# Performance work log

Measured on AMD Instinct MI355X. Metric: run time of the kernel, lower is better.

The kernel has to match this reference:

```python
import jax, jax.numpy as jnp
import numpy as np

B, N, H, V, STEP = 16, 50, 128, 40000, 2

def setup_inputs() -> dict:
    key = jax.random.key(0)
    ks = jax.random.split(key, 24)
    def nrm(i, shape, s=0.08):
        return jax.random.normal(ks[i], shape, jnp.float32) * s
    items = jax.random.randint(ks[0], (B, N), 0, V)
    A = jax.random.uniform(ks[1], (B, N, 2 * N), jnp.float32)
    lengths = jax.random.randint(ks[2], (B,), 1, N + 1)
    mask = (jnp.arange(N)[None, :] < lengths[:, None]).astype(jnp.int32)
    emb = nrm(3, (V, H), 0.1).at[0].set(0.0)  # padding_idx=0 row zeroed
    return dict(
        items=items, A=A, mask=mask, emb=emb,
        w_ih=nrm(4, (3 * H, 2 * H)), w_hh=nrm(5, (3 * H, H)),
        b_ih=nrm(6, (3 * H,)), b_hh=nrm(7, (3 * H,)),
        b_iah=nrm(8, (H,)), b_oah=nrm(9, (H,)),
        W_ein=nrm(10, (H, H)), b_ein=nrm(11, (H,)),
        W_eout=nrm(12, (H, H)), b_eout=nrm(13, (H,)),
        W_one=nrm(14, (H, H)), b_one=nrm(15, (H,)),
        W_two=nrm(16, (H, H)), b_two=nrm(17, (H,)),
        w_three=nrm(18, (H,)),
        W_tr=nrm(19, (H, 2 * H)), b_tr=nrm(20, (H,)),
        W_t=nrm(21, (H, H)),
    )

def gnn_cell(A, hidden, w_ih, w_hh, b_ih, b_hh, b_iah, b_oah, W_ein, b_ein, W_eout, b_eout):
    # A: [B,N,2N], hidden: [B,N,H]
    ein = hidden @ W_ein.T + b_ein
    eout = hidden @ W_eout.T + b_eout
    input_in = jnp.einsum('bnm,bmh->bnh', A[:, :, :N], ein) + b_iah
    input_out = jnp.einsum('bnm,bmh->bnh', A[:, :, N:], eout) + b_oah
    inputs = jnp.concatenate([input_in, input_out], axis=-1)  # [B,N,2H]
    gi = inputs @ w_ih.T + b_ih
    gh = hidden @ w_hh.T + b_hh
    i_r, i_i, i_n = jnp.split(gi, 3, axis=-1)
    h_r, h_i, h_n = jnp.split(gh, 3, axis=-1)
    resetgate = jax.nn.sigmoid(i_r + h_r)
    inputgate = jax.nn.sigmoid(i_i + h_i)
    newgate = jnp.tanh(i_n + resetgate * h_n)
    return newgate + inputgate * (hidden - newgate)

def reference(items, A, mask, emb, w_ih, w_hh, b_ih, b_hh, b_iah, b_oah,
              W_ein, b_ein, W_eout, b_eout, W_one, b_one, W_two, b_two,
              w_three, W_tr, b_tr, W_t):
    hidden = emb[items]  # [B,N,H]
    for _ in range(STEP):
        hidden = gnn_cell(A, hidden, w_ih, w_hh, b_ih, b_hh, b_iah, b_oah,
                          W_ein, b_ein, W_eout, b_eout)
    # compute_scores
    lengths = jnp.sum(mask, axis=1)  # all >= 1 by construction
    ht = hidden[jnp.arange(B), lengths - 1]  # [B,H] last valid item
    q1 = (ht @ W_one.T + b_one)[:, None, :]
    q2 = hidden @ W_two.T + b_two
    mexp = mask[..., None].astype(jnp.float32)  # [B,N,1]
    alpha_logits = jax.nn.sigmoid(q1 + q2) @ w_three[:, None]  # [B,N,1]
    alpha = jax.nn.softmax(jnp.where(mexp == 0, -jnp.inf, alpha_logits), axis=1)
    a = jnp.sum(alpha * hidden * mexp, axis=1)  # [B,H]
    a = jnp.concatenate([a, ht], axis=1) @ W_tr.T + b_tr  # hybrid (nonhybrid=False)
    b_emb = emb[1:]  # [V-1,H]
    qt = (hidden * mexp) @ W_t.T  # [B,N,H]
    beta_logits = jnp.einsum('vh,bnh->bvn', b_emb, qt)
    beta_logits = jnp.where(mask[:, None, :] == 0, -jnp.inf, beta_logits)
    beta = jax.nn.softmax(beta_logits, axis=-1)  # [B,V-1,N]
    target = jnp.einsum('bvn,bnh->bvh', beta, qt * mexp)  # [B,V-1,H]
    # scores = sum((a[:,None,:] + target) * b_emb, -1), split to avoid extra buffer
    scores = jnp.einsum('bvh,vh->bv', target, b_emb) + a @ b_emb.T
    return scores  # [B, V-1]
```

## Files before the change

### kernel.cpp

```cpp
#include <hip/hip_runtime.h>

#define BB 16
#define NN 50
#define HH 128
#define VV 40000
#define VO 39999

typedef unsigned short u16;
typedef unsigned int u32;
typedef __attribute__((ext_vector_type(8))) short short8;
typedef __attribute__((ext_vector_type(4))) float f32x4;

#define OFF_HID    0
#define OFF_HID2   102400
#define OFF_Q2     102400
#define OFF_Q1     204800
#define OFF_HT     206848
#define OFF_QTBF   307200
#define OFF_LEN    411648
#define OFF_WTWOT  591888
#define OFF_WTT    608272
#define OFF_WONET  624656
#define OFF_WTRT   641040

__device__ __forceinline__ float sigm(float x){ return 1.0f/(1.0f+__expf(-x)); }
__device__ __forceinline__ float b2f(u16 u){
  union { u32 i; float f; } c; c.i = ((u32)u) << 16; return c.f;
}
__device__ __forceinline__ u16 f2b(float f){
  union { float f; u32 i; } c; c.f = f;
  u32 u = c.i;
  return (u16)((u + 0x7fffu + ((u >> 16) & 1u)) >> 16);
}
__device__ __forceinline__ int frag_idx(int b, int n, int k){
  int tile = n>>4, vlo = n&15, kc = k>>5, quad = (k>>3)&3, j = k&7;
  return (((b*4+tile)*4+kc)<<9) + ((quad<<4)+vlo)*8 + j;
}

__global__ void k_pre(const int* __restrict__ items, const float* __restrict__ emb,
                      const float* __restrict__ W_two, const float* __restrict__ W_t,
                      const float* __restrict__ W_one, const float* __restrict__ W_tr,
                      float* __restrict__ ws){
  int idx = blockIdx.x*256 + threadIdx.x;
  if (idx < 102400){
    int r = idx >> 7, h = idx & 127;
    ws[OFF_HID + idx] = emb[items[r]*128 + h];
  } else if (idx < 118784){
    int i = idx-102400; int k=i>>7, h=i&127;
    ws[OFF_WTWOT + i] = W_two[h*128 + k];
  } else if (idx < 135168){
    int i = idx-118784; int k=i>>7, h=i&127;
    ws[OFF_WTT + i] = W_t[h*128 + k];
  } else if (idx < 151552){
    int i = idx-135168; int k=i>>7, h=i&127;
    ws[OFF_WONET + i] = W_one[h*128 + k];
  } else if (idx < 184320){
    int i = idx-151552; int k=i>>7, h=i&127;
    ws[OFF_WTRT + i] = W_tr[h*256 + k];
  }
}

__global__ void __launch_bounds__(384) k_step(const float* __restrict__ A,
                       const float* __restrict__ w_ih, const float* __restrict__ w_hh,
                       const float* __restrict__ W_ein, const float* __restrict__ W_eout,
                       const float* __restrict__ b_ein, const float* __restrict__ b_eout,
                       const float* __restrict__ b_iah, const float* __restrict__ b_oah,
                       const float* __restrict__ b_ih, const float* __restrict__ b_hh,
                       float* __restrict__ ws, int srcOff, int dstOff){
  __shared__ float hall[50][128];
  __shared__ float arow[2][104];
  __shared__ float hAl[2][256];
  __shared__ float sAl[2][2];
  __shared__ float inp[2][256];
  __shared__ float gil[2][384];
  __shared__ float ghl[2][384];
  int t = threadIdx.x;
  int tile = blockIdx.x, b = blockIdx.y;
  int n0 = tile*2;
  const float* hsrc = ws + srcOff + b*6400;
  for (int o=t; o<1600; o+=384) ((float4*)hall)[o] = ((const float4*)hsrc)[o];
  for (int o=t; o<208; o+=384){
    int r=o/104, c=o-r*104;
    arow[r][c] = (c<100) ? A[(size_t)(b*NN+n0+r)*100 + c] : 0.0f;
  }
  __syncthreads();
  for (int o=t; o<512; o+=384){
    int r = o>>8, kk = o&255;
    int k = kk & 127;
    const float* ar = &arow[r][(kk>>7)*50];
    float acc = 0.0f;
    #pragma unroll 5
    for (int m=0;m<50;m++) acc += ar[m]*hall[m][k];
    hAl[r][kk] = acc;
  }
  if (t < 4){
    int r = t>>1, half = t&1;
    const float* ar = &arow[r][half*50];
    float s = 0.0f;
    for (int m=0;m<50;m++) s += ar[m];
    sAl[r][half] = s;
  }
  __syncthreads();
  for (int o=t; o<512; o+=384){
    int r = o>>8, c8 = o&255;
    int in_half = (c8 < 128);
    int c = c8 & 127;
    const float* wrow = (in_half ? W_ein : W_eout) + c*128;
    const float* hv = &hAl[r][in_half ? 0 : 128];
    float acc = in_half ? (b_iah[c] + sAl[r][0]*b_ein[c])
                        : (b_oah[c] + sAl[r][1]*b_eout[c]);
    #pragma unroll 8
    for (int k=0;k<128;k+=4){
      float4 w4 = *(const float4*)(wrow + k);
      float4 h4 = *(const float4*)(hv + k);
      acc += h4.x*w4.x + h4.y*w4.y + h4.z*w4.z + h4.w*w4.w;
    }
    inp[r][c8] = acc;
  }
  __syncthreads();
  {
    int j = t;
    float gi0=b_ih[j], gi1=gi0, gh0=b_hh[j], gh1=gh0;
    const float* wi = w_ih + j*256;
    const float* wh = w_hh + j*128;
    #pragma unroll 8
    for (int k=0;k<256;k+=4){
      float4 w4 = *(const float4*)(wi + k);
      float4 i0 = *(const float4*)(&inp[0][k]);
      float4 i1 = *(const float4*)(&inp[1][k]);
      gi0 += i0.x*w4.x + i0.y*w4.y + i0.z*w4.z + i0.w*w4.w;
      gi1 += i1.x*w4.x + i1.y*w4.y + i1.z*w4.z + i1.w*w4.w;
    }
    #pragma unroll 8
    for (int k=0;k<128;k+=4){
      float4 w4 = *(const float4*)(wh + k);
      float4 h0 = *(const float4*)(&hall[n0][k]);
      float4 h1 = *(const float4*)(&hall[n0+1][k]);
      gh0 += h0.x*w4.x + h0.y*w4.y + h0.z*w4.z + h0.w*w4.w;
      gh1 += h1.x*w4.x + h1.y*w4.y + h1.z*w4.z + h1.w*w4.w;
    }
    gil[0][j]=gi0; gil[1][j]=gi1; ghl[0][j]=gh0; ghl[1][j]=gh1;
  }
  __syncthreads();
  if (t < 256){
    int r=t>>7, h=t&127, row=n0+r;
    float ir_=gil[r][h], ii=gil[r][128+h], inw=gil[r][256+h];
    float hr_=ghl[r][h], hi2=ghl[r][128+h], hn=ghl[r][256+h];
    float rg=sigm(ir_+hr_), ig=sigm(ii+hi2), ng=tanhf(inw+rg*hn);
    float hv=hall[row][h];
    ws[dstOff + (b*NN+row)*128 + h] = ng + ig*(hv-ng);
  }
}

__global__ void __launch_bounds__(256) k_post(const int* __restrict__ mask,
                      const float* __restrict__ b_two, const float* __restrict__ b_one,
                      float* __restrict__ ws){
  int bx = blockIdx.x, t = threadIdx.x;
  u16* qtbf = (u16*)(ws + OFF_QTBF);
  if (bx < 200){
    bool isq2 = bx < 100;
    int r0 = (isq2 ? bx : bx-100) * 8;
    __shared__ float hl[1024];
    for (int i=0;i<4;i++) hl[t+i*256] = ws[OFF_HID + r0*128 + t + i*256];
    __syncthreads();
    int h = t & 127, g = t >> 7;
    const float* wT = ws + (isq2 ? OFF_WTWOT : OFF_WTT);
    float binit = isq2 ? b_two[h] : 0.0f;
    float acc[4];
    #pragma unroll
    for (int r=0;r<4;r++) acc[r] = binit;
    for (int k4=0;k4<32;k4++){
      int k = k4*4;
      float w0 = wT[(k+0)*128+h], w1 = wT[(k+1)*128+h];
      float w2 = wT[(k+2)*128+h], w3 = wT[(k+3)*128+h];
      #pragma unroll
      for (int r=0;r<4;r++){
        float4 hv = *(const float4*)(hl + (g*4+r)*128 + k);
        acc[r] += hv.x*w0 + hv.y*w1 + hv.z*w2 + hv.w*w3;
      }
    }
    #pragma unroll
    for (int r=0;r<4;r++){
      int row = r0 + g*4 + r;
      if (isq2) ws[OFF_Q2 + row*128 + h] = acc[r];
      else {
        float val = mask[row] ? acc[r] : 0.0f;
        int b = row/NN, n = row - b*NN;
        qtbf[frag_idx(b, n, h)] = f2b(val);
      }
    }
  } else if (bx < 248){
    int i = (bx-200)*256 + t;
    #pragma unroll
    for (int kk=0;kk<2;kk++){
      int e = i*2 + kk;
      int b = e/1536, rem = e - b*1536;
      int kc = rem/384, rem2 = rem - kc*384;
      int quad = rem2/96, vv = rem2 - quad*96;
      int vlo = 4 + vv/8, j = vv & 7;
      qtbf[(((b*4+3)*4+kc)<<9) + ((quad<<4)+vlo)*8 + j] = 0;
    }
  } else {
    __shared__ float htl[128];
    int b = bx - 248;
    if (t < 128){
      int len = 0;
      for (int n=0;n<NN;n++) len += mask[b*NN+n];
      if (len<1) len=1; if (len>NN) len=NN;
      float ht = ws[OFF_HID + (b*NN + len-1)*128 + t];
      ws[OFF_HT + b*128 + t] = ht;
      htl[t] = ht;
      if (t==0) ((int*)(ws+OFF_LEN))[b] = len;
    }
    __syncthreads();
    if (t < 128){
      const float* w1T = ws + OFF_WONET;
      float q1 = b_one[t];
      for (int k=0;k<128;k+=4){
        float4 h4 = *(const float4*)(htl + k);
        q1 += h4.x*w1T[(k+0)*128+t] + h4.y*w1T[(k+1)*128+t]
            + h4.z*w1T[(k+2)*128+t] + h4.w*w1T[(k+3)*128+t];
      }
      ws[OFF_Q1 + b*128 + t] = q1;
    }
  }
}

__global__ void __launch_bounds__(256) k_attn2(const float* __restrict__ w_three,
                        const float* __restrict__ b_tr, float* __restrict__ ws){
  __shared__ float q2l[NN*129];
  __shared__ float q1l[128], w3l[128], htl[128], al[128], pt2[128], alg[64];
  int t = threadIdx.x;
  int b = blockIdx.x;
  for (int o=t;o<6400;o+=256){ int n=o>>7, h=o&127; q2l[n*129+h] = ws[OFF_Q2 + b*6400 + o]; }
  if (t < 128){
    q1l[t] = ws[OFF_Q1 + b*128 + t];
    w3l[t] = w_three[t];
    htl[t] = ws[OFF_HT + b*128 + t];
  }
  int len = ((const int*)(ws+OFF_LEN))[b];
  __syncthreads();
  if (t < 200){
    int n = t>>2, part = t&3;
    if (n < len){
      const float* qr  = q2l + n*129 + part*32;
      const float* q1p = q1l + part*32;
      const float* w3p = w3l + part*32;
      float s = 0.0f;
      for (int h=0;h<32;h++) s += w3p[h]*sigm(q1p[h]+qr[h]);
      s += __shfl_xor(s,1); s += __shfl_xor(s,2);
      if (part==0) alg[n] = s;
    }
  }
  __syncthreads();
  if (t < 64){
    float v = (t<len) ? alg[t] : -1e30f;
    float m = v;
    m = fmaxf(m, __shfl_xor(m,1));  m = fmaxf(m, __shfl_xor(m,2));
    m = fmaxf(m, __shfl_xor(m,4));  m = fmaxf(m, __shfl_xor(m,8));
    m = fmaxf(m, __shfl_xor(m,16)); m = fmaxf(m, __shfl_xor(m,32));
    float e = (t<len) ? __expf(v - m) : 0.0f;
    float ss = e;
    ss += __shfl_xor(ss,1);  ss += __shfl_xor(ss,2);
    ss += __shfl_xor(ss,4);  ss += __shfl_xor(ss,8);
    ss += __shfl_xor(ss,16); ss += __shfl_xor(ss,32);
    float inv = 1.0f/ss;
    if (t<len) alg[t] = e*inv;
  }
  __syncthreads();
  if (t < 128){
    const float* hid = ws + OFF_HID + b*6400;
    float a = 0.0f;
    for (int n=0;n<len;n++) a += alg[n]*hid[n*128+t];
    al[t] = a;
  }
  __syncthreads();
  float p1 = 0.0f;
  if (t < 256){
    int g2 = t>>7, h = t&127;
    const float* wtr = ws + OFF_WTRT + g2*128*128;
    const float* src = g2 ? htl : al;
    float p = 0.0f;
    for (int k=0;k<128;k++) p += src[k]*wtr[k*128+h];
    if (g2) pt2[h] = p; else p1 = p;
  }
  __syncthreads();
  if (t < 128){
    float af = b_tr[t] + p1 + pt2[t];
    u16 hi = f2b(af);
    u16 lo = f2b(af - b2f(hi));
    u16* qtbf = (u16*)(ws + OFF_QTBF);
    qtbf[frag_idx(b, 50, t)] = hi;
    qtbf[frag_idx(b, 51, t)] = lo;
  }
}

__global__ void __launch_bounds__(256) k_scores(const float* __restrict__ emb,
                                                const float* __restrict__ ws,
                                                float* __restrict__ out){
  __shared__ u16 qlds[8192];
  int tid = threadIdx.x;
  int lane = tid & 63, wave = tid >> 6;
  int quad = lane >> 4, vlo = lane & 15;
  int v = blockIdx.y*64 + wave*16 + vlo;
  int vc = (v < VO) ? v : (VO-1);
  const float* erow = emb + (size_t)(vc+1)*128;
  short8 bfr[4];
  #pragma unroll
  for (int kc=0;kc<4;kc++){
    const float4* p = (const float4*)(erow + kc*32 + quad*8);
    float4 x = p[0], y = p[1];
    union { short8 s; u32 w[4]; } u;
    u.w[0] = (u32)f2b(x.x) | ((u32)f2b(x.y)<<16);
    u.w[1] = (u32)f2b(x.z) | ((u32)f2b(x.w)<<16);
    u.w[2] = (u32)f2b(y.x) | ((u32)f2b(y.y)<<16);
    u.w[3] = (u32)f2b(y.z) | ((u32)f2b(y.w)<<16);
    bfr[kc] = u.s;
  }
  const u16* qtf = (const u16*)(ws + OFF_QTBF);
  const int* slen = (const int*)(ws + OFF_LEN);
  int b0 = blockIdx.x*4;
  for (int bi=0;bi<4;bi++){
    int b = b0 + bi;
    __syncthreads();
    {
      const uint4* src = (const uint4*)qtf + (size_t)b*1024;
      uint4* dst = (uint4*)qlds;
      #pragma unroll
      for (int r=0;r<4;r++) dst[tid + r*256] = src[tid + r*256];
    }
    __syncthreads();
    int len = slen[b];
    f32x4 acc0={0.f,0.f,0.f,0.f}, acc1=acc0, acc2=acc0, acc3=acc0;
    #pragma unroll
    for (int kc=0;kc<4;kc++){
      const u16* base = qlds + kc*512 + lane*8;
      short8 a0 = *(const short8*)(base + 0*2048);
      short8 a1 = *(const short8*)(base + 1*2048);
      short8 a2 = *(const short8*)(base + 2*2048);
      short8 a3 = *(const short8*)(base + 3*2048);
      acc0 = __builtin_amdgcn_mfma_f32_16x16x32_bf16(a0, bfr[kc], acc0, 0,0,0);
      acc1 = __builtin_amdgcn_mfma_f32_16x16x32_bf16(a1, bfr[kc], acc1, 0,0,0);
      acc2 = __builtin_amdgcn_mfma_f32_16x16x32_bf16(a2, bfr[kc], acc2, 0,0,0);
      acc3 = __builtin_amdgcn_mfma_f32_16x16x32_bf16(a3, bfr[kc], acc3, 0,0,0);
    }
    int nb = quad*4;
    float ss=0.f, nm=0.f;
    #pragma unroll
    for (int r=0;r<4;r++){
      { int n=nb+r;    if(n<len){ float e=__expf(acc0[r]); ss+=e; nm+=e*acc0[r]; } }
      { int n=nb+r+16; if(n<len){ float e=__expf(acc1[r]); ss+=e; nm+=e*acc1[r]; } }
      { int n=nb+r+32; if(n<len){ float e=__expf(acc2[r]); ss+=e; nm+=e*acc2[r]; } }
      { int n=nb+r+48; if(n<len){ float e=__expf(acc3[r]); ss+=e; nm+=e*acc3[r]; } }
    }
    ss += __shfl_xor(ss,16); ss += __shfl_xor(ss,32);
    nm += __shfl_xor(nm,16); nm += __shfl_xor(nm,32);
    if (quad==0 && v < VO){
      float pa = acc3[2] + acc3[3];
      out[(size_t)b*VO + v] = nm/ss + pa;
    }
  }
}

extern "C" void kernel_launch(void* const* d_in, const int* in_sizes, int n_in,
                              void* d_out, int out_size, void* d_ws, size_t ws_size,
                              hipStream_t stream){
  const int*   items  = (const int*)d_in[0];
  const float* A      = (const float*)d_in[1];
  const int*   mask   = (const int*)d_in[2];
  const float* emb    = (const float*)d_in[3];
  const float* w_ih   = (const float*)d_in[4];
  const float* w_hh   = (const float*)d_in[5];
  const float* b_ih   = (const float*)d_in[6];
  const float* b_hh   = (const float*)d_in[7];
  const float* b_iah  = (const float*)d_in[8];
  const float* b_oah  = (const float*)d_in[9];
  const float* W_ein  = (const float*)d_in[10];
  const float* b_ein  = (const float*)d_in[11];
  const float* W_eout = (const float*)d_in[12];
  const float* b_eout = (const float*)d_in[13];
  const float* W_one  = (const float*)d_in[14];
  const float* b_one  = (const float*)d_in[15];
  const float* W_two  = (const float*)d_in[16];
  const float* b_two  = (const float*)d_in[17];
  const float* w_three= (const float*)d_in[18];
  const float* W_tr   = (const float*)d_in[19];
  const float* b_tr   = (const float*)d_in[20];
  const float* W_t    = (const float*)d_in[21];
  float* ws  = (float*)d_ws;
  float* out = (float*)d_out;

  k_pre<<<720,256,0,stream>>>(items,emb,W_two,W_t,W_one,W_tr,ws);
  k_step<<<dim3(25,16),384,0,stream>>>(A,w_ih,w_hh,W_ein,W_eout,b_ein,b_eout,b_iah,b_oah,b_ih,b_hh,ws,OFF_HID,OFF_HID2);
  k_step<<<dim3(25,16),384,0,stream>>>(A,w_ih,w_hh,W_ein,W_eout,b_ein,b_eout,b_iah,b_oah,b_ih,b_hh,ws,OFF_HID2,OFF_HID);
  k_post<<<264,256,0,stream>>>(mask,b_two,b_one,ws);
  k_attn2<<<16,256,0,stream>>>(w_three,b_tr,ws);
  k_scores<<<dim3(4,625),256,0,stream>>>(emb,ws,out);
}
```

Before: 261.9 us.

## Split GNN step into A-aggregation and gate kernels with 4-row weight reuse

Each GNN step is split into two kernels. k_ha computes A·hidden aggregates for 4 rows per block and writes them to the workspace. k_gates then processes 4 rows per block using transposed weights for coalesced loads and LDS-tiled w_ih, so each weight fetch is reused across 4 rows instead of 2. This cuts redundant weight traffic in the step kernels, at the cost of two extra launches, a workspace round trip for the aggregates, and a larger preprocessing kernel.

```diff
diff --git a/kernel.cpp b/kernel.cpp
--- a/kernel.cpp
+++ b/kernel.cpp
@@ -16,12 +16,17 @@
 #define OFF_Q2     102400
 #define OFF_Q1     204800
 #define OFF_HT     206848
+#define OFF_WTWOT  208896
+#define OFF_WTT    225280
+#define OFF_WONET  241664
+#define OFF_WTRT   258048
+#define OFF_WEINT  290816
 #define OFF_QTBF   307200
+#define OFF_WEOUTT 372736
 #define OFF_LEN    411648
-#define OFF_WTWOT  591888
-#define OFF_WTT    608272
-#define OFF_WONET  624656
-#define OFF_WTRT   641040
+#define OFF_HA     411664
+#define OFF_WHHT   616464
+#define OFF_HASUM  665616
 
 __device__ __forceinline__ float sigm(float x){ return 1.0f/(1.0f+__expf(-x)); }
 __device__ __forceinline__ float b2f(u16 u){
@@ -40,7 +45,8 @@
 __global__ void k_pre(const int* __restrict__ items, const float* __restrict__ emb,
                       const float* __restrict__ W_two, const float* __restrict__ W_t,
                       const float* __restrict__ W_one, const float* __restrict__ W_tr,
-                      float* __restrict__ ws){
+                      const float* __restrict__ W_ein, const float* __restrict__ W_eout,
+                      const float* __restrict__ w_hh, float* __restrict__ ws){
   int idx = blockIdx.x*256 + threadIdx.x;
   if (idx < 102400){
     int r = idx >> 7, h = idx & 127;
@@ -57,98 +63,145 @@
   } else if (idx < 184320){
     int i = idx-151552; int k=i>>7, h=i&127;
     ws[OFF_WTRT + i] = W_tr[h*256 + k];
-  }
-}
-
-__global__ void __launch_bounds__(384) k_step(const float* __restrict__ A,
-                       const float* __restrict__ w_ih, const float* __restrict__ w_hh,
-                       const float* __restrict__ W_ein, const float* __restrict__ W_eout,
+  } else if (idx < 200704){
+    int i = idx-184320; int k=i>>7, h=i&127;
+    ws[OFF_WEINT + i] = W_ein[h*128 + k];
+  } else if (idx < 217088){
+    int i = idx-200704; int k=i>>7, h=i&127;
+    ws[OFF_WEOUTT + i] = W_eout[h*128 + k];
+  } else if (idx < 266240){
+    int i = idx-217088; int k=i/384, j=i-k*384;
+    ws[OFF_WHHT + i] = w_hh[j*128 + k];
+  }
+}
+
+__global__ void __launch_bounds__(384) k_ha(const float* __restrict__ A,
+                       float* __restrict__ ws, int srcOff){
+  __shared__ float hall[50][128];
+  __shared__ float arow[4][104];
+  int t = threadIdx.x;
+  int tile = blockIdx.x, b = blockIdx.y;
+  int n0 = tile*4;
+  const float* hsrc = ws + srcOff + b*6400;
+  for (int o=t; o<1600; o+=384) ((float4*)hall)[o] = ((const float4*)hsrc)[o];
+  for (int o=t; o<416; o+=384){
+    int r=o/104, c=o-r*104;
+    arow[r][c] = (c<100 && n0+r<NN) ? A[(size_t)(b*NN+n0+r)*100 + c] : 0.0f;
+  }
+  __syncthreads();
+  for (int o=t; o<1024; o+=384){
+    int r = o>>8, kk = o&255;
+    int row = n0 + r;
+    if (row < NN){
+      int k = kk & 127;
+      const float* ar = &arow[r][(kk>>7)*50];
+      float acc = 0.0f;
+      #pragma unroll 5
+      for (int m=0;m<50;m++) acc += ar[m]*hall[m][k];
+      ws[OFF_HA + (size_t)(b*NN+row)*256 + kk] = acc;
+    }
+  }
+  if (t < 8){
+    int r = t>>1, half = t&1;
+    if (n0+r < NN){
+      const float* ar = &arow[r][half*50];
+      float s = 0.0f;
+      for (int m=0;m<50;m++) s += ar[m];
+      ws[OFF_HASUM + (b*NN+n0+r)*2 + half] = s;
+    }
+  }
+}
+
+__global__ void __launch_bounds__(512) k_gates(const float* __restrict__ w_ih,
                        const float* __restrict__ b_ein, const float* __restrict__ b_eout,
                        const float* __restrict__ b_iah, const float* __restrict__ b_oah,
                        const float* __restrict__ b_ih, const float* __restrict__ b_hh,
                        float* __restrict__ ws, int srcOff, int dstOff){
-  __shared__ float hall[50][128];
-  __shared__ float arow[2][104];
-  __shared__ float hAl[2][256];
-  __shared__ float sAl[2][2];
-  __shared__ float inp[2][256];
-  __shared__ float gil[2][384];
-  __shared__ float ghl[2][384];
+  __shared__ float h4[4][128];
+  __shared__ float ha4[4][256];
+  __shared__ float sa4[4][2];
+  __shared__ float inp4[4][256];
+  __shared__ float gil[4][384];
+  __shared__ float ghl[4][384];
+  __shared__ float wtile[16][384];
   int t = threadIdx.x;
-  int tile = blockIdx.x, b = blockIdx.y;
-  int n0 = tile*2;
-  const float* hsrc = ws + srcOff + b*6400;
-  for (int o=t; o<1600; o+=384) ((float4*)hall)[o] = ((const float4*)hsrc)[o];
-  for (int o=t; o<208; o+=384){
-    int r=o/104, c=o-r*104;
-    arow[r][c] = (c<100) ? A[(size_t)(b*NN+n0+r)*100 + c] : 0.0f;
-  }
-  __syncthreads();
-  for (int o=t; o<512; o+=384){
-    int r = o>>8, kk = o&255;
-    int k = kk & 127;
-    const float* ar = &arow[r][(kk>>7)*50];
-    float acc = 0.0f;
-    #pragma unroll 5
-    for (int m=0;m<50;m++) acc += ar[m]*hall[m][k];
-    hAl[r][kk] = acc;
-  }
-  if (t < 4){
-    int r = t>>1, half = t&1;
-    const float* ar = &arow[r][half*50];
-    float s = 0.0f;
-    for (int m=0;m<50;m++) s += ar[m];
-    sAl[r][half] = s;
-  }
-  __syncthreads();
-  for (int o=t; o<512; o+=384){
-    int r = o>>8, c8 = o&255;
-    int in_half = (c8 < 128);
+  int g0 = blockIdx.x*4;
+  h4[t>>7][t&127] = ws[srcOff + g0*128 + t];
+  ha4[t>>8][t&255] = ws[OFF_HA + g0*256 + t];
+  { int o2 = t+512; ha4[o2>>8][o2&255] = ws[OFF_HA + g0*256 + o2]; }
+  if (t < 8) sa4[t>>1][t&1] = ws[OFF_HASUM + g0*2 + t];
+  __syncthreads();
+  {
+    int c8 = t & 255, rb = t >> 8;
+    int in_half = (c8 < 128) ? 1 : 0;
     int c = c8 & 127;
-    const float* wrow = (in_half ? W_ein : W_eout) + c*128;
-    const float* hv = &hAl[r][in_half ? 0 : 128];
-    float acc = in_half ? (b_iah[c] + sAl[r][0]*b_ein[c])
-                        : (b_oah[c] + sAl[r][1]*b_eout[c]);
-    #pragma unroll 8
+    const float* wT = ws + (in_half ? OFF_WEINT : OFF_WEOUTT) + c;
+    const float* haA = &ha4[rb][in_half ? 0 : 128];
+    const float* haB = &ha4[rb+2][in_half ? 0 : 128];
+    float a0 = in_half ? (b_iah[c] + sa4[rb  ][0]*b_ein[c]) : (b_oah[c] + sa4[rb  ][1]*b_eout[c]);
+    float a1 = in_half ? (b_iah[c] + sa4[rb+2][0]*b_ein[c]) : (b_oah[c] + sa4[rb+2][1]*b_eout[c]);
     for (int k=0;k<128;k+=4){
-      float4 w4 = *(const float4*)(wrow + k);
-      float4 h4 = *(const float4*)(hv + k);
-      acc += h4.x*w4.x + h4.y*w4.y + h4.z*w4.z + h4.w*w4.w;
-    }
-    inp[r][c8] = acc;
+      float w0=wT[(k+0)*128], w1=wT[(k+1)*128], w2=wT[(k+2)*128], w3=wT[(k+3)*128];
+      float4 hA = *(const float4*)(haA + k);
+      float4 hB = *(const float4*)(haB + k);
+      a0 += hA.x*w0 + hA.y*w1 + hA.z*w2 + hA.w*w3;
+      a1 += hB.x*w0 + hB.y*w1 + hB.z*w2 + hB.w*w3;
+    }
+    inp4[rb][c8] = a0;
+    inp4[rb+2][c8] = a1;
+  }
+  __syncthreads();
+  int j = t;
+  float gacc0=0,gacc1=0,gacc2=0,gacc3=0;
+  if (j < 384){ float bi = b_ih[j]; gacc0=gacc1=gacc2=gacc3=bi; }
+  for (int k0=0;k0<256;k0+=16){
+    #pragma unroll
+    for (int q=0;q<3;q++){
+      int u = t + q*512;
+      int row = u>>2, seg = u&3;
+      float4 v = *(const float4*)(w_ih + row*256 + k0 + seg*4);
+      int kb = seg*4;
+      wtile[kb+0][row]=v.x; wtile[kb+1][row]=v.y; wtile[kb+2][row]=v.z; wtile[kb+3][row]=v.w;
+    }
+    __syncthreads();
+    if (j < 384){
+      #pragma unroll
+      for (int kk=0;kk<16;kk++){
+        float w = wtile[kk][j];
+        gacc0 += w*inp4[0][k0+kk];
+        gacc1 += w*inp4[1][k0+kk];
+        gacc2 += w*inp4[2][k0+kk];
+        gacc3 += w*inp4[3][k0+kk];
+      }
+    }
+    __syncthreads();
+  }
+  if (j < 384){ gil[0][j]=gacc0; gil[1][j]=gacc1; gil[2][j]=gacc2; gil[3][j]=gacc3; }
+  if (j < 384){
+    float bh = b_hh[j];
+    float q0=bh,q1=bh,q2=bh,q3=bh;
+    const float* wT = ws + OFF_WHHT + j;
+    for (int k=0;k<128;k+=4){
+      float w0=wT[(k+0)*384], w1=wT[(k+1)*384], w2=wT[(k+2)*384], w3=wT[(k+3)*384];
+      float4 v0 = *(const float4*)(&h4[0][k]);
+      float4 v1 = *(const float4*)(&h4[1][k]);
+      float4 v2 = *(const float4*)(&h4[2][k]);
+      float4 v3 = *(const float4*)(&h4[3][k]);
+      q0 += v0.x*w0 + v0.y*w1 + v0.z*w2 + v0.w*w3;
+      q1 += v1.x*w0 + v1.y*w1 + v1.z*w2 + v1.w*w3;
+      q2 += v2.x*w0 + v2.y*w1 + v2.z*w2 + v2.w*w3;
+      q3 += v3.x*w0 + v3.y*w1 + v3.z*w2 + v3.w*w3;
+    }
+    ghl[0][j]=q0; ghl[1][j]=q1; ghl[2][j]=q2; ghl[3][j]=q3;
   }
   __syncthreads();
   {
-    int j = t;
-    float gi0=b_ih[j], gi1=gi0, gh0=b_hh[j], gh1=gh0;
-    const float* wi = w_ih + j*256;
-    const float* wh = w_hh + j*128;
-    #pragma unroll 8
-    for (int k=0;k<256;k+=4){
-      float4 w4 = *(const float4*)(wi + k);
-      float4 i0 = *(const float4*)(&inp[0][k]);
-      float4 i1 = *(const float4*)(&inp[1][k]);
-      gi0 += i0.x*w4.x + i0.y*w4.y + i0.z*w4.z + i0.w*w4.w;
-      gi1 += i1.x*w4.x + i1.y*w4.y + i1.z*w4.z + i1.w*w4.w;
-    }
-    #pragma unroll 8
-    for (int k=0;k<128;k+=4){
-      float4 w4 = *(const float4*)(wh + k);
-      float4 h0 = *(const float4*)(&hall[n0][k]);
-      float4 h1 = *(const float4*)(&hall[n0+1][k]);
-      gh0 += h0.x*w4.x + h0.y*w4.y + h0.z*w4.z + h0.w*w4.w;
-      gh1 += h1.x*w4.x + h1.y*w4.y + h1.z*w4.z + h1.w*w4.w;
-    }
-    gil[0][j]=gi0; gil[1][j]=gi1; ghl[0][j]=gh0; ghl[1][j]=gh1;
-  }
-  __syncthreads();
-  if (t < 256){
-    int r=t>>7, h=t&127, row=n0+r;
+    int r = t>>7, h = t&127;
     float ir_=gil[r][h], ii=gil[r][128+h], inw=gil[r][256+h];
     float hr_=ghl[r][h], hi2=ghl[r][128+h], hn=ghl[r][256+h];
     float rg=sigm(ir_+hr_), ig=sigm(ii+hi2), ng=tanhf(inw+rg*hn);
-    float hv=hall[row][h];
-    ws[dstOff + (b*NN+row)*128 + h] = ng + ig*(hv-ng);
+    float hv=h4[r][h];
+    ws[dstOff + (g0+r)*128 + h] = ng + ig*(hv-ng);
   }
 }
 
@@ -217,9 +270,9 @@
       const float* w1T = ws + OFF_WONET;
       float q1 = b_one[t];
       for (int k=0;k<128;k+=4){
-        float4 h4 = *(const float4*)(htl + k);
-        q1 += h4.x*w1T[(k+0)*128+t] + h4.y*w1T[(k+1)*128+t]
-            + h4.z*w1T[(k+2)*128+t] + h4.w*w1T[(k+3)*128+t];
+        float4 h4v = *(const float4*)(htl + k);
+        q1 += h4v.x*w1T[(k+0)*128+t] + h4v.y*w1T[(k+1)*128+t]
+            + h4v.z*w1T[(k+2)*128+t] + h4v.w*w1T[(k+3)*128+t];
       }
       ws[OFF_Q1 + b*128 + t] = q1;
     }
@@ -390,10 +443,12 @@
   float* ws  = (float*)d_ws;
   float* out = (float*)d_out;
 
-  k_pre<<<720,256,0,stream>>>(items,emb,W_two,W_t,W_one,W_tr,ws);
-  k_step<<<dim3(25,16),384,0,stream>>>(A,w_ih,w_hh,W_ein,W_eout,b_ein,b_eout,b_iah,b_oah,b_ih,b_hh,ws,OFF_HID,OFF_HID2);
-  k_step<<<dim3(25,16),384,0,stream>>>(A,w_ih,w_hh,W_ein,W_eout,b_ein,b_eout,b_iah,b_oah,b_ih,b_hh,ws,OFF_HID2,OFF_HID);
-  k_post<<<264,256,0,stream>>>(mask,b_two,b_one,ws);
+  k_pre<<<1040,256,0,stream>>>(items,emb,W_two,W_t,W_one,W_tr,W_ein,W_eout,w_hh,ws);
+  k_ha   <<<dim3(13,16),384,0,stream>>>(A,ws,OFF_HID);
+  k_gates<<<200,512,0,stream>>>(w_ih,b_ein,b_eout,b_iah,b_oah,b_ih,b_hh,ws,OFF_HID,OFF_HID2);
+  k_ha   <<<dim3(13,16),384,0,stream>>>(A,ws,OFF_HID2);
+  k_gates<<<200,512,0,stream>>>(w_ih,b_ein,b_eout,b_iah,b_oah,b_ih,b_hh,ws,OFF_HID2,OFF_HID);
+  k_post <<<264,256,0,stream>>>(mask,b_two,b_one,ws);
   k_attn2<<<16,256,0,stream>>>(w_three,b_tr,ws);
   k_scores<<<dim3(4,625),256,0,stream>>>(emb,ws,out);
 }
```

Measured after the change: 218.9 us. 16.4% less time.
